# Performance work log

Measured on AMD Instinct MI355X. Metric: run time of the kernel, lower is better.

## Reference

```python
import jax, jax.numpy as jnp
import numpy as np

V = 50257; E = 1024; H = 1024; L = 256; NL = 2; D = 10


def setup_inputs() -> dict:
    key = jax.random.key(0)
    ks = jax.random.split(key, 16)
    n = lambda k, s: jax.random.normal(k, s, dtype=jnp.float32)
    return {
        "input_tok": jax.random.randint(ks[0], (1, 1), 0, V),
        "h0": n(ks[1], (NL, 1, H)),
        "c0": n(ks[2], (NL, 1, H)),
        "h_s": n(ks[3], (L, 1, H)),
        "h_t_tilde": n(ks[4], (1, 1, H)),
        "emb": n(ks[5], (V, E)) * 0.02,
        "Wp": n(ks[6], (H, H)) * (H ** -0.5),
        "wdot": n(ks[7], (1, H)) * (H ** -0.5),
        "Wbil": n(ks[8], (1, H, H)) * (H ** -0.5),
        "Wcomb": n(ks[9], (H, 2 * H)) * ((2 * H) ** -0.5),
        "bcomb": jnp.zeros((H,), jnp.float32),
        "Wih0": n(ks[10], (4 * H, E + H)) * ((E + H) ** -0.5),
        "Whh0": n(ks[11], (4 * H, H)) * (H ** -0.5),
        "bih0": jnp.zeros((4 * H,), jnp.float32),
        "bhh0": jnp.zeros((4 * H,), jnp.float32),
        "Wih1": n(ks[12], (4 * H, H)) * (H ** -0.5),
        "Whh1": n(ks[13], (4 * H, H)) * (H ** -0.5),
        "bih1": jnp.zeros((4 * H,), jnp.float32),
        "bhh1": jnp.zeros((4 * H,), jnp.float32),
        "Wout": n(ks[14], (V, H)) * (H ** -0.5),
        "bout": jnp.zeros((V,), jnp.float32),
    }


def _lstm_cell(x, h, c, Wih, Whh, bih, bhh):
    # torch LSTM gate order: i, f, g, o
    g = x @ Wih.T + bih + h @ Whh.T + bhh
    i, f, gg, o = jnp.split(g, 4, axis=-1)
    c2 = jax.nn.sigmoid(f) * c + jax.nn.sigmoid(i) * jnp.tanh(gg)
    h2 = jax.nn.sigmoid(o) * jnp.tanh(c2)
    return h2, c2


def reference(input_tok, h0, c0, h_s, h_t_tilde, emb, Wp, wdot, Wbil, Wcomb, bcomb,
              Wih0, Whh0, bih0, bhh0, Wih1, Whh1, bih1, bhh1, Wout, bout):
    embedding = emb[input_tok]                                  # [1,1,E]
    x = jnp.concatenate((embedding, h_t_tilde), axis=-1)[0]     # [1,E+H]
    h1, c1 = _lstm_cell(x, h0[0], c0[0], Wih0, Whh0, bih0, bhh0)
    h2, c2 = _lstm_cell(h1, h0[1], c0[1], Wih1, Whh1, bih1, bhh1)
    h_new = jnp.stack((h1, h2)); c_new = jnp.stack((c1, c2))
    h_t = h2                                                    # [1,H]
    Ls = h_s.shape[0]
    p_t = Ls * jax.nn.sigmoid(jnp.tanh(h_t @ Wp.T) @ wdot.T).squeeze()  # scalar
    s = jnp.round(p_t).astype(jnp.int32)
    idx = jnp.arange(Ls)
    lo = jnp.maximum(s - D, 0); hi = jnp.minimum(s + D, Ls - 1)
    mask = (idx >= lo) & (idx <= hi)                            # [L] local window
    # bilinear score h_t^T W h_s over all positions; mask outside window
    score = jnp.einsum('bh,ohk,lbk->lbo', h_t, Wbil, h_s)       # [L,1,1]
    neg = jnp.finfo(score.dtype).min
    a = jax.nn.softmax(jnp.where(mask[:, None, None], score, neg), axis=0)
    # NOTE: original uses exp(+d^2/(D/2)^2) (no minus sign); replicated faithfully.
    expo = jnp.where(mask, ((idx.astype(jnp.float32) - p_t) ** 2) / ((D / 2) ** 2), 0.0)
    a_t = a * jnp.exp(expo)[:, None, None]                      # [L,1,1]
    win = (hi - lo + 1).astype(jnp.float32)
    context = jnp.sum(a_t * h_s, axis=0, keepdims=True) / win   # [1,1,H] (mean over window)
    cat = jnp.concatenate((context, h_t[None]), axis=-1)        # [1,1,2H]
    h_t_tilde_new = jnp.tanh(cat @ Wcomb.T + bcomb)             # [1,1,H]
    y = jax.nn.log_softmax(h_t_tilde_new @ Wout.T + bout, axis=-1)  # [1,1,V]
    return (y, h_new, c_new, h_t_tilde_new, a_t, p_t)
```

## Files before the change

### kernel.cpp

```cpp
#include <hip/hip_runtime.h>
#include <math.h>

#define V 50257
#define E 1024
#define HH 1024
#define LL 256

#define O_H  (V)
#define O_C  (V + 2*HH)
#define O_HT (V + 4*HH)
#define O_A  (V + 5*HH)
#define O_P  (V + 5*HH + LL)

#define W_T    0
#define W_V    1024
#define W_H1   2048
#define W_H2   3072
#define W_Z    4096
#define W_BS   54400

#define NBL   2048

__device__ __forceinline__ float sigmoidf_(float x) { return 1.f / (1.f + expf(-x)); }
__device__ __forceinline__ float dot4(float4 a, float4 b) {
    return a.x * b.x + a.y * b.y + a.z * b.z + a.w * b.w;
}

__device__ __forceinline__ float block_sum(float v, float* red) {
    int lane = threadIdx.x & 63, wv = threadIdx.x >> 6;
#pragma unroll
    for (int o = 32; o > 0; o >>= 1) v += __shfl_down(v, o, 64);
    __syncthreads();
    if (lane == 0) red[wv] = v;
    __syncthreads();
    return red[0] + red[1] + red[2] + red[3];
}

__global__ __launch_bounds__(512) void k_lstmA(
    const float* __restrict__ Wih0, const float* __restrict__ Whh0,
    const float* __restrict__ Whh1,
    const float* __restrict__ bih0, const float* __restrict__ bhh0,
    const float* __restrict__ emb, const int* __restrict__ tok,
    const float* __restrict__ htt,
    const float* __restrict__ h0, const float* __restrict__ c0,
    float* __restrict__ h1o, float* __restrict__ c1o, float* __restrict__ h1w,
    float* __restrict__ p1, float* __restrict__ vzero) {
    const int u = blockIdx.x, tid = threadIdx.x;
    if (tid == 0) vzero[u] = 0.f;
    const float4* xa4 = (const float4*)(emb + (size_t)tok[0] * E);
    const float4* xb4 = (const float4*)htt;
    const float4* r0 = (const float4*)(Wih0 + (size_t)u * 2048);
    const float4* r1 = (const float4*)(Wih0 + (size_t)(u + HH) * 2048);
    const float4* r2 = (const float4*)(Wih0 + (size_t)(u + 2*HH) * 2048);
    const float4* r3 = (const float4*)(Wih0 + (size_t)(u + 3*HH) * 2048);
    float4 xv = (tid < 256) ? xa4[tid] : xb4[tid - 256];
    float a0 = dot4(r0[tid], xv), a1 = dot4(r1[tid], xv);
    float a2 = dot4(r2[tid], xv), a3 = dot4(r3[tid], xv);
    float b0 = 0.f, b1 = 0.f, b2 = 0.f, b3 = 0.f;
    if (tid < 256) {
        const float4* s0 = (const float4*)(Whh0 + (size_t)u * HH);
        const float4* s1 = (const float4*)(Whh0 + (size_t)(u + HH) * HH);
        const float4* s2 = (const float4*)(Whh0 + (size_t)(u + 2*HH) * HH);
        const float4* s3 = (const float4*)(Whh0 + (size_t)(u + 3*HH) * HH);
        float4 hv = ((const float4*)h0)[tid];
        a0 += dot4(s0[tid], hv); a1 += dot4(s1[tid], hv);
        a2 += dot4(s2[tid], hv); a3 += dot4(s3[tid], hv);
    } else {
        int j = tid - 256;
        const float4* t0 = (const float4*)(Whh1 + (size_t)u * HH);
        const float4* t1 = (const float4*)(Whh1 + (size_t)(u + HH) * HH);
        const float4* t2 = (const float4*)(Whh1 + (size_t)(u + 2*HH) * HH);
        const float4* t3 = (const float4*)(Whh1 + (size_t)(u + 3*HH) * HH);
        float4 gv = ((const float4*)(h0 + HH))[j];
        b0 = dot4(t0[j], gv); b1 = dot4(t1[j], gv);
        b2 = dot4(t2[j], gv); b3 = dot4(t3[j], gv);
    }
    const int lane = tid & 63, wv = tid >> 6;
#pragma unroll
    for (int o = 32; o > 0; o >>= 1) {
        a0 += __shfl_down(a0, o, 64); a1 += __shfl_down(a1, o, 64);
        a2 += __shfl_down(a2, o, 64); a3 += __shfl_down(a3, o, 64);
        b0 += __shfl_down(b0, o, 64); b1 += __shfl_down(b1, o, 64);
        b2 += __shfl_down(b2, o, 64); b3 += __shfl_down(b3, o, 64);
    }
    __shared__ float sma[8][4], smb[8][4];
    if (lane == 0) {
        sma[wv][0] = a0; sma[wv][1] = a1; sma[wv][2] = a2; sma[wv][3] = a3;
        smb[wv][0] = b0; smb[wv][1] = b1; smb[wv][2] = b2; smb[wv][3] = b3;
    }
    __syncthreads();
    if (tid == 0) {
        float g[4], p[4];
#pragma unroll
        for (int i = 0; i < 4; ++i) {
            float ga = 0.f, pb = 0.f;
#pragma unroll
            for (int w = 0; w < 8; ++w) { ga += sma[w][i]; pb += smb[w][i]; }
            g[i] = ga + bih0[u + i*HH] + bhh0[u + i*HH];
            p[i] = pb;
        }
        float c = sigmoidf_(g[1]) * c0[u] + sigmoidf_(g[0]) * tanhf(g[2]);
        float h = sigmoidf_(g[3]) * tanhf(c);
        h1o[u] = h; c1o[u] = c; h1w[u] = h;
        p1[u*4+0] = p[0]; p1[u*4+1] = p[1]; p1[u*4+2] = p[2]; p1[u*4+3] = p[3];
    }
}

__global__ void k_lstmB(
    const float* __restrict__ Wih1,
    const float* __restrict__ bih1, const float* __restrict__ bhh1,
    const float* __restrict__ h1w, const float* __restrict__ p1,
    const float* __restrict__ h0, const float* __restrict__ c0,
    float* __restrict__ h2o, float* __restrict__ c2o, float* __restrict__ h2w) {
    const int u = blockIdx.x, tid = threadIdx.x;
    const float4* r0 = (const float4*)(Wih1 + (size_t)u * HH);
    const float4* r1 = (const float4*)(Wih1 + (size_t)(u + HH) * HH);
    const float4* r2 = (const float4*)(Wih1 + (size_t)(u + 2*HH) * HH);
    const float4* r3 = (const float4*)(Wih1 + (size_t)(u + 3*HH) * HH);
    float4 hv = ((const float4*)h1w)[tid];
    float a0 = dot4(r0[tid], hv), a1 = dot4(r1[tid], hv);
    float a2 = dot4(r2[tid], hv), a3 = dot4(r3[tid], hv);
    const int lane = tid & 63, wv = tid >> 6;
#pragma unroll
    for (int o = 32; o > 0; o >>= 1) {
        a0 += __shfl_down(a0, o, 64); a1 += __shfl_down(a1, o, 64);
        a2 += __shfl_down(a2, o, 64); a3 += __shfl_down(a3, o, 64);
    }
    __shared__ float sm[4][4];
    if (lane == 0) { sm[wv][0] = a0; sm[wv][1] = a1; sm[wv][2] = a2; sm[wv][3] = a3; }
    __syncthreads();
    if (tid == 0) {
        float g[4];
#pragma unroll
        for (int i = 0; i < 4; ++i)
            g[i] = sm[0][i] + sm[1][i] + sm[2][i] + sm[3][i]
                 + p1[u*4+i] + bih1[u + i*HH] + bhh1[u + i*HH];
        float c = sigmoidf_(g[1]) * c0[HH + u] + sigmoidf_(g[0]) * tanhf(g[2]);
        float h = sigmoidf_(g[3]) * tanhf(c);
        h2o[u] = h; c2o[u] = c; h2w[u] = h;
    }
}

__global__ void k_ptv(const float* __restrict__ Wp, const float* __restrict__ Wbil,
                      const float* __restrict__ h2, float* __restrict__ t_out,
                      float* __restrict__ v_out) {
    __shared__ float red[4];
    if (blockIdx.x < HH) {
        int r = blockIdx.x;
        const float4* row = (const float4*)(Wp + (size_t)r * HH);
        const float4* h24 = (const float4*)h2;
        float acc = dot4(row[threadIdx.x], h24[threadIdx.x]);
        float tot = block_sum(acc, red);
        if (threadIdx.x == 0) t_out[r] = tanhf(tot);
    } else {
        int b = blockIdx.x - HH;
        int h0 = b * 32;
        int k4 = threadIdx.x;
        const float4* W4 = (const float4*)Wbil;
        float4 acc = make_float4(0.f, 0.f, 0.f, 0.f);
        for (int h = h0; h < h0 + 32; ++h) {
            float hv = h2[h];
            float4 w = W4[(size_t)h * 256 + k4];
            acc.x += hv * w.x; acc.y += hv * w.y;
            acc.z += hv * w.z; acc.w += hv * w.w;
        }
        atomicAdd(&v_out[k4 * 4 + 0], acc.x);
        atomicAdd(&v_out[k4 * 4 + 1], acc.y);
        atomicAdd(&v_out[k4 * 4 + 2], acc.z);
        atomicAdd(&v_out[k4 * 4 + 3], acc.w);
    }
}

__global__ void k_combattn(const float* __restrict__ wdot, const float* __restrict__ t,
                           const float* __restrict__ v, const float* __restrict__ hs,
                           const float* __restrict__ h2, const float* __restrict__ Wcomb,
                           const float* __restrict__ bcomb,
                           float* __restrict__ outv, float* __restrict__ outv2,
                           float* __restrict__ ato, float* __restrict__ pto) {
    const int u = blockIdx.x, tid = threadIdx.x;
    const int lane = tid & 63, wv = tid >> 6;
    __shared__ float red[4];
    __shared__ float ssc[32];
    __shared__ float sa[LL];
    float p;
    {
        const float4* w4 = (const float4*)wdot;
        const float4* t4 = (const float4*)t;
        float acc = dot4(w4[tid], t4[tid]);
        p = (float)LL * sigmoidf_(block_sum(acc, red));
    }
    if (u == 0 && tid == 0) pto[0] = p;
    const int si = (int)rintf(p);
    const int lo = max(si - 10, 0), hi = min(si + 10, LL - 1);
    const int W = hi - lo + 1;
    const float4* v4 = (const float4*)v;
    for (int l = lo + wv; l <= hi; l += 4) {
        const float4* row = (const float4*)(hs + (size_t)l * HH);
        float a = 0.f;
#pragma unroll
        for (int j = lane; j < 256; j += 64) a += dot4(row[j], v4[j]);
#pragma unroll
        for (int o = 32; o > 0; o >>= 1) a += __shfl_xor(a, o, 64);
        if (lane == 0) ssc[l - lo] = a;
    }
    __syncthreads();
    float M = -INFINITY;
    for (int i = 0; i < W; ++i) M = fmaxf(M, ssc[i]);
    float S = 0.f;
    for (int i = 0; i < W; ++i) S += expf(ssc[i] - M);
    {
        bool mask = (tid >= lo) && (tid <= hi);
        int wi = min(max(tid - lo, 0), 31);
        float e = mask ? expf(ssc[wi] - M) : 0.f;
        float d = (float)tid - p;
        float at = mask ? (e / S) * expf(d * d * 0.04f) : 0.f;
        sa[tid] = at;
        if (u == 0) ato[tid] = at;
    }
    __syncthreads();
    const float4* hs4 = (const float4*)hs;
    float4 c = make_float4(0.f, 0.f, 0.f, 0.f);
    for (int l = lo; l <= hi; ++l) {
        float a = sa[l];
        float4 hv = hs4[(size_t)l * 256 + tid];
        c.x += a * hv.x; c.y += a * hv.y; c.z += a * hv.z; c.w += a * hv.w;
    }
    const float inv_win = 1.f / (float)W;
    c.x *= inv_win; c.y *= inv_win; c.z *= inv_win; c.w *= inv_win;
    {
        const float4* row = (const float4*)(Wcomb + (size_t)u * (2 * HH));
        const float4* h24 = (const float4*)h2;
        float acc = dot4(row[tid], c) + dot4(row[256 + tid], h24[tid]);
        float tot = block_sum(acc, red);
        if (tid == 0) {
            float h = tanhf(tot + bcomb[u]);
            outv[u] = h; outv2[u] = h;
        }
    }
}

__global__ void k_logits(const float* __restrict__ Wout, const float* __restrict__ bout,
                         const float* __restrict__ x, float* __restrict__ z,
                         float* __restrict__ bsum) {
    const int b = blockIdx.x, tid = threadIdx.x;
    const int lane = tid & 63, wvi = tid >> 6;
    const int start = b * 24 + min(b, 1105);
    const int cnt = 24 + (b < 1105 ? 1 : 0);
    const int rend = start + cnt;
    const float4* x4 = (const float4*)x;
    float4 x0 = x4[lane], x1 = x4[lane + 64], x2 = x4[lane + 128], x3 = x4[lane + 192];
    float s = 0.f;
    int r = start + wvi;
    float4 c0, c1, c2, c3;
    bool has = r < rend;
    if (has) {
        const float4* rp = (const float4*)(Wout + (size_t)r * 1024) + lane;
        c0 = rp[0]; c1 = rp[64]; c2 = rp[128]; c3 = rp[192];
    }
    while (has) {
        const int rn = r + 4;
        const bool hasn = rn < rend;
        float4 n0, n1, n2, n3;
        if (hasn) {
            const float4* np = (const float4*)(Wout + (size_t)rn * 1024) + lane;
            n0 = np[0]; n1 = np[64]; n2 = np[128]; n3 = np[192];
        }
        float acc = dot4(c0, x0) + dot4(c1, x1) + dot4(c2, x2) + dot4(c3, x3);
#pragma unroll
        for (int o = 32; o > 0; o >>= 1) acc += __shfl_xor(acc, o, 64);
        float zz = acc + bout[r];
        if (lane == 0) z[r] = zz;
        s += expf(zz);
        r = rn; has = hasn;
        c0 = n0; c1 = n1; c2 = n2; c3 = n3;
    }
    __shared__ float wsv[4];
    if (lane == 0) wsv[wvi] = s;
    __syncthreads();
    if (tid == 0) bsum[b] = wsv[0] + wsv[1] + wsv[2] + wsv[3];
}

__global__ void k_sub(const float* __restrict__ z, const float* __restrict__ bsum,
                      float* __restrict__ y) {
    const int tid = threadIdx.x;
    __shared__ float red[4];
    __shared__ float lzs;
    float s = 0.f;
    for (int i = tid; i < NBL; i += 256) s += bsum[i];
    float S = block_sum(s, red);
    if (tid == 0) lzs = logf(S);
    __syncthreads();
    const float lz = lzs;
    int i = blockIdx.x * 256 + tid;
    if (i < V) y[i] = z[i] - lz;
}

extern "C" void kernel_launch(void* const* d_in, const int* in_sizes, int n_in,
                              void* d_out, int out_size, void* d_ws, size_t ws_size,
                              hipStream_t stream) {
    const int*   tok   = (const int*)  d_in[0];
    const float* h0    = (const float*)d_in[1];
    const float* c0    = (const float*)d_in[2];
    const float* hs    = (const float*)d_in[3];
    const float* htt   = (const float*)d_in[4];
    const float* emb   = (const float*)d_in[5];
    const float* Wp    = (const float*)d_in[6];
    const float* wdot  = (const float*)d_in[7];
    const float* Wbil  = (const float*)d_in[8];
    const float* Wcomb = (const float*)d_in[9];
    const float* bcomb = (const float*)d_in[10];
    const float* Wih0  = (const float*)d_in[11];
    const float* Whh0  = (const float*)d_in[12];
    const float* bih0  = (const float*)d_in[13];
    const float* bhh0  = (const float*)d_in[14];
    const float* Wih1  = (const float*)d_in[15];
    const float* Whh1  = (const float*)d_in[16];
    const float* bih1  = (const float*)d_in[17];
    const float* bhh1  = (const float*)d_in[18];
    const float* Wout  = (const float*)d_in[19];
    const float* bout  = (const float*)d_in[20];

    float* out = (float*)d_out;
    float* ws  = (float*)d_ws;

    float* h1o  = out + O_H;
    float* h2o  = out + O_H + HH;
    float* c1o  = out + O_C;
    float* c2o  = out + O_C + HH;
    float* htto = out + O_HT;
    float* ato  = out + O_A;
    float* pto  = out + O_P;
    float* p1   = out;

    hipLaunchKernelGGL(k_lstmA, dim3(1024), dim3(512), 0, stream,
                       Wih0, Whh0, Whh1, bih0, bhh0, emb, tok, htt, h0, c0,
                       h1o, c1o, ws + W_H1, p1, ws + W_V);
    hipLaunchKernelGGL(k_lstmB, dim3(1024), dim3(256), 0, stream,
                       Wih1, bih1, bhh1, ws + W_H1, p1, h0, c0,
                       h2o, c2o, ws + W_H2);
    hipLaunchKernelGGL(k_ptv, dim3(1024 + 32), dim3(256), 0, stream,
                       Wp, Wbil, ws + W_H2, ws + W_T, ws + W_V);
    hipLaunchKernelGGL(k_combattn, dim3(1024), dim3(256), 0, stream,
                       wdot, ws + W_T, ws + W_V, hs, ws + W_H2, Wcomb, bcomb,
                       htto, ws + W_H1, ato, pto);
    hipLaunchKernelGGL(k_logits, dim3(NBL), dim3(256), 0, stream,
                       Wout, bout, ws + W_H1, ws + W_Z, ws + W_BS);
    hipLaunchKernelGGL(k_sub, dim3((V + 255) / 256), dim3(256), 0, stream,
                       ws + W_Z, ws + W_BS, out);
}
```

Before: 85.47 us.

## Widen LSTM layer-1 blocks and stride logits rows across 8192 waves

k_lstmB now runs 512 threads per block, with each half of the block computing two of the four gate dot products, so twice as many waves stream Wih1. k_logits drops the contiguous per-block row ranges and the software-prefetch loop. It launches 1024 blocks of 8 waves, and each wave handles up to 7 rows strided by 8192. This is meant to raise memory-level parallelism and even out row balance on the memory-bound GEMVs, at the cost of losing the explicit double-buffered prefetch.

```diff
diff --git a/kernel.cpp b/kernel.cpp
--- a/kernel.cpp
+++ b/kernel.cpp
@@ -19,7 +19,8 @@
 #define W_Z    4096
 #define W_BS   54400
 
-#define NBL   2048
+#define NWL   8192
+#define MAXR  7
 
 __device__ __forceinline__ float sigmoidf_(float x) { return 1.f / (1.f + expf(-x)); }
 __device__ __forceinline__ float dot4(float4 a, float4 b) {
@@ -106,35 +107,36 @@
     }
 }
 
-__global__ void k_lstmB(
+__global__ __launch_bounds__(512) void k_lstmB(
     const float* __restrict__ Wih1,
     const float* __restrict__ bih1, const float* __restrict__ bhh1,
     const float* __restrict__ h1w, const float* __restrict__ p1,
     const float* __restrict__ h0, const float* __restrict__ c0,
     float* __restrict__ h2o, float* __restrict__ c2o, float* __restrict__ h2w) {
     const int u = blockIdx.x, tid = threadIdx.x;
-    const float4* r0 = (const float4*)(Wih1 + (size_t)u * HH);
-    const float4* r1 = (const float4*)(Wih1 + (size_t)(u + HH) * HH);
-    const float4* r2 = (const float4*)(Wih1 + (size_t)(u + 2*HH) * HH);
-    const float4* r3 = (const float4*)(Wih1 + (size_t)(u + 3*HH) * HH);
-    float4 hv = ((const float4*)h1w)[tid];
-    float a0 = dot4(r0[tid], hv), a1 = dot4(r1[tid], hv);
-    float a2 = dot4(r2[tid], hv), a3 = dot4(r3[tid], hv);
+    const int j = tid & 255, half = tid >> 8;
+    const int ra = u + (2 * half) * HH;
+    const float4* pa = (const float4*)(Wih1 + (size_t)ra * HH);
+    const float4* pb = (const float4*)(Wih1 + (size_t)(ra + HH) * HH);
+    float4 hv = ((const float4*)h1w)[j];
+    float a = dot4(pa[j], hv), b = dot4(pb[j], hv);
     const int lane = tid & 63, wv = tid >> 6;
 #pragma unroll
     for (int o = 32; o > 0; o >>= 1) {
-        a0 += __shfl_down(a0, o, 64); a1 += __shfl_down(a1, o, 64);
-        a2 += __shfl_down(a2, o, 64); a3 += __shfl_down(a3, o, 64);
-    }
-    __shared__ float sm[4][4];
-    if (lane == 0) { sm[wv][0] = a0; sm[wv][1] = a1; sm[wv][2] = a2; sm[wv][3] = a3; }
+        a += __shfl_down(a, o, 64); b += __shfl_down(b, o, 64);
+    }
+    __shared__ float sm[8][2];
+    if (lane == 0) { sm[wv][0] = a; sm[wv][1] = b; }
     __syncthreads();
     if (tid == 0) {
         float g[4];
+        g[0] = sm[0][0] + sm[1][0] + sm[2][0] + sm[3][0];
+        g[1] = sm[0][1] + sm[1][1] + sm[2][1] + sm[3][1];
+        g[2] = sm[4][0] + sm[5][0] + sm[6][0] + sm[7][0];
+        g[3] = sm[4][1] + sm[5][1] + sm[6][1] + sm[7][1];
 #pragma unroll
         for (int i = 0; i < 4; ++i)
-            g[i] = sm[0][i] + sm[1][i] + sm[2][i] + sm[3][i]
-                 + p1[u*4+i] + bih1[u + i*HH] + bhh1[u + i*HH];
+            g[i] += p1[u*4+i] + bih1[u + i*HH] + bhh1[u + i*HH];
         float c = sigmoidf_(g[1]) * c0[HH + u] + sigmoidf_(g[0]) * tanhf(g[2]);
         float h = sigmoidf_(g[3]) * tanhf(c);
         h2o[u] = h; c2o[u] = c; h2w[u] = h;
@@ -239,45 +241,37 @@
     }
 }
 
-__global__ void k_logits(const float* __restrict__ Wout, const float* __restrict__ bout,
-                         const float* __restrict__ x, float* __restrict__ z,
-                         float* __restrict__ bsum) {
-    const int b = blockIdx.x, tid = threadIdx.x;
-    const int lane = tid & 63, wvi = tid >> 6;
-    const int start = b * 24 + min(b, 1105);
-    const int cnt = 24 + (b < 1105 ? 1 : 0);
-    const int rend = start + cnt;
+__global__ __launch_bounds__(512) void k_logits(
+    const float* __restrict__ Wout, const float* __restrict__ bout,
+    const float* __restrict__ x, float* __restrict__ z,
+    float* __restrict__ bsum) {
+    const int tid = threadIdx.x, lane = tid & 63, wvi = tid >> 6;
+    const int w = blockIdx.x * 8 + wvi;
     const float4* x4 = (const float4*)x;
     float4 x0 = x4[lane], x1 = x4[lane + 64], x2 = x4[lane + 128], x3 = x4[lane + 192];
     float s = 0.f;
-    int r = start + wvi;
-    float4 c0, c1, c2, c3;
-    bool has = r < rend;
-    if (has) {
-        const float4* rp = (const float4*)(Wout + (size_t)r * 1024) + lane;
-        c0 = rp[0]; c1 = rp[64]; c2 = rp[128]; c3 = rp[192];
-    }
-    while (has) {
-        const int rn = r + 4;
-        const bool hasn = rn < rend;
-        float4 n0, n1, n2, n3;
-        if (hasn) {
-            const float4* np = (const float4*)(Wout + (size_t)rn * 1024) + lane;
-            n0 = np[0]; n1 = np[64]; n2 = np[128]; n3 = np[192];
+    for (int i = 0; i < MAXR; ++i) {
+        int r = w + i * NWL;
+        if (r < V) {
+            const float4* row = (const float4*)(Wout + (size_t)r * 1024) + lane;
+            float acc = dot4(row[0], x0) + dot4(row[64], x1)
+                      + dot4(row[128], x2) + dot4(row[192], x3);
+#pragma unroll
+            for (int o = 32; o > 0; o >>= 1) acc += __shfl_xor(acc, o, 64);
+            float zz = acc + bout[r];
+            if (lane == 0) z[r] = zz;
+            s += expf(zz);
         }
-        float acc = dot4(c0, x0) + dot4(c1, x1) + dot4(c2, x2) + dot4(c3, x3);
-#pragma unroll
-        for (int o = 32; o > 0; o >>= 1) acc += __shfl_xor(acc, o, 64);
-        float zz = acc + bout[r];
-        if (lane == 0) z[r] = zz;
-        s += expf(zz);
-        r = rn; has = hasn;
-        c0 = n0; c1 = n1; c2 = n2; c3 = n3;
-    }
-    __shared__ float wsv[4];
+    }
+    __shared__ float wsv[8];
     if (lane == 0) wsv[wvi] = s;
     __syncthreads();
-    if (tid == 0) bsum[b] = wsv[0] + wsv[1] + wsv[2] + wsv[3];
+    if (tid == 0) {
+        float S = 0.f;
+#pragma unroll
+        for (int q = 0; q < 8; ++q) S += wsv[q];
+        bsum[blockIdx.x] = S;
+    }
 }
 
 __global__ void k_sub(const float* __restrict__ z, const float* __restrict__ bsum,
@@ -286,7 +280,7 @@
     __shared__ float red[4];
     __shared__ float lzs;
     float s = 0.f;
-    for (int i = tid; i < NBL; i += 256) s += bsum[i];
+    for (int i = tid; i < 1024; i += 256) s += bsum[i];
     float S = block_sum(s, red);
     if (tid == 0) lzs = logf(S);
     __syncthreads();
@@ -335,7 +329,7 @@
     hipLaunchKernelGGL(k_lstmA, dim3(1024), dim3(512), 0, stream,
                        Wih0, Whh0, Whh1, bih0, bhh0, emb, tok, htt, h0, c0,
                        h1o, c1o, ws + W_H1, p1, ws + W_V);
-    hipLaunchKernelGGL(k_lstmB, dim3(1024), dim3(256), 0, stream,
+    hipLaunchKernelGGL(k_lstmB, dim3(1024), dim3(512), 0, stream,
                        Wih1, bih1, bhh1, ws + W_H1, p1, h0, c0,
                        h2o, c2o, ws + W_H2);
     hipLaunchKernelGGL(k_ptv, dim3(1024 + 32), dim3(256), 0, stream,
@@ -343,7 +337,7 @@
     hipLaunchKernelGGL(k_combattn, dim3(1024), dim3(256), 0, stream,
                        wdot, ws + W_T, ws + W_V, hs, ws + W_H2, Wcomb, bcomb,
                        htto, ws + W_H1, ato, pto);
-    hipLaunchKernelGGL(k_logits, dim3(NBL), dim3(256), 0, stream,
+    hipLaunchKernelGGL(k_logits, dim3(1024), dim3(512), 0, stream,
                        Wout, bout, ws + W_H1, ws + W_Z, ws + W_BS);
     hipLaunchKernelGGL(k_sub, dim3((V + 255) / 256), dim3(256), 0, stream,
                        ws + W_Z, ws + W_BS, out);
```

After: 82.72 us. 1.03x faster.
